# Performance work log

Measured on AMD Instinct MI355X. Metric: run time of the kernel, lower is better.

## Reference

```python
import jax, jax.numpy as jnp
import numpy as np

B, S, D = 4, 2048, 1024
H = 16
HD = D // H  # 64
FF = 4096


def setup_inputs() -> dict:
    key = jax.random.key(0)
    ks = jax.random.split(key, 11)
    sd = 1.0 / np.sqrt(D)
    inp = {
        "embeddings": jax.random.normal(ks[0], (B, S, D), dtype=jnp.float32),
        # per-head Linear weights stacked: [H, head_dim, D] (torch Linear layout)
        "Wq": jax.random.uniform(ks[1], (H, HD, D), jnp.float32, -sd, sd),
        "bq": jax.random.uniform(ks[2], (H, HD), jnp.float32, -sd, sd),
        "Wk": jax.random.uniform(ks[3], (H, HD, D), jnp.float32, -sd, sd),
        "bk": jax.random.uniform(ks[4], (H, HD), jnp.float32, -sd, sd),
        "Wv": jax.random.uniform(ks[5], (H, HD, D), jnp.float32, -sd, sd),
        "bv": jax.random.uniform(ks[6], (H, HD), jnp.float32, -sd, sd),
        "W1": jax.random.uniform(ks[7], (FF, D), jnp.float32, -sd, sd),
        "b1": jax.random.uniform(ks[8], (FF,), jnp.float32, -sd, sd),
        "W2": jax.random.uniform(ks[9], (D, FF), jnp.float32, -1.0 / np.sqrt(FF), 1.0 / np.sqrt(FF)),
        "b2": jax.random.uniform(ks[10], (D,), jnp.float32, -1.0 / np.sqrt(FF), 1.0 / np.sqrt(FF)),
    }
    return inp


def reference(embeddings, Wq, bq, Wk, bk, Wv, bv, W1, b1, W2, b2):
    # Per-head projections, batched over heads: [B,H,S,HD]
    Q = jnp.einsum("bsd,hed->bhse", embeddings, Wq) + bq[None, :, None, :]
    K = jnp.einsum("bsd,hed->bhse", embeddings, Wk) + bk[None, :, None, :]
    V = jnp.einsum("bsd,hed->bhse", embeddings, Wv) + bv[None, :, None, :]
    # NOTE: original scales by sqrt(embed_dim), not sqrt(head_dim)
    scale = 1.0 / jnp.sqrt(jnp.asarray(D, embeddings.dtype))
    scores = jnp.einsum("bhse,bhte->bhst", Q, K) * scale  # [B,H,S,S]
    A = jax.nn.softmax(scores, axis=-1)
    Hh = jnp.einsum("bhst,bhte->bhse", A, V)  # [B,H,S,HD]
    # concat heads along last dim (head order matches torch.cat)
    Hcat = jnp.transpose(Hh, (0, 2, 1, 3)).reshape(B, S, D)
    hid = jax.nn.relu(Hcat @ W1.T + b1)
    return hid @ W2.T + b2
```

## Files before the change

kernel.cpp:

```cpp
#include <hip/hip_runtime.h>
#include <stdint.h>


typedef __attribute__((ext_vector_type(8))) short bf16x8;
typedef __attribute__((ext_vector_type(4))) float f32x4;

__device__ __forceinline__ float bf2f(unsigned short u) {
  union { float f; uint32_t i; } v; v.i = ((uint32_t)u) << 16; return v.f;
}
__device__ __forceinline__ unsigned short f2bf(float f) {
  union { float f; uint32_t i; } v; v.f = f;
  uint32_t i = v.i;
  return (unsigned short)((i + 0x7fffu + ((i >> 16) & 1u)) >> 16);
}

#if __has_builtin(__builtin_amdgcn_exp2f)
#define EXP2(x) __builtin_amdgcn_exp2f(x)
#else
#define EXP2(x) __expf((x) * 0.6931471805599453f)
#endif

__device__ __forceinline__ uint32_t cvtpk(float p0, float p1) {
  uint32_t r;
  asm("v_cvt_pk_bf16_f32 %0, %1, %2" : "=v"(r) : "v"(p0), "v"(p1));
  return r;
}

__device__ __forceinline__ void gld16(const void* g, void* l) {
  __builtin_amdgcn_global_load_lds(
      (const __attribute__((address_space(1))) uint32_t*)(uintptr_t)g,
      (__attribute__((address_space(3))) uint32_t*)(uintptr_t)l, 16, 0, 0);
}

#define SCALE_Q 0.04508422002778011f

#define W1B          0
#define W2B    4194304
#define B1B    8388608
#define B2B    8392704
#define BQB    8393728
#define BKB    8394752
#define BVB    8395776
#define EMBB   8396800
#define WQB   16785408
#define WKB   17833984
#define WVB   18882560
#define QOFF  19931136
#define KOFF  28319744
#define VTOFF 36708352
#define HCOFF 45096960
#define HIDOFF 8396800

__global__ void cvt_all(const float* __restrict__ emb, const float* __restrict__ Wq,
                        const float* __restrict__ bq,  const float* __restrict__ Wk,
                        const float* __restrict__ bk,  const float* __restrict__ Wv,
                        const float* __restrict__ bv,  const float* __restrict__ W1,
                        const float* __restrict__ b1,  const float* __restrict__ W2,
                        const float* __restrict__ b2,  unsigned short* __restrict__ ws) {
  const int i4 = blockIdx.x * 256 + threadIdx.x;
  if (i4 >= 4982784) return;
  const float* s; unsigned short* d; int base;
  if      (i4 < 2097152) { s = emb; d = ws + EMBB; base = 0; }
  else if (i4 < 2359296) { s = Wq;  d = ws + WQB;  base = 2097152; }
  else if (i4 < 2621440) { s = Wk;  d = ws + WKB;  base = 2359296; }
  else if (i4 < 2883584) { s = Wv;  d = ws + WVB;  base = 2621440; }
  else if (i4 < 3932160) { s = W1;  d = ws + W1B;  base = 2883584; }
  else if (i4 < 4980736) { s = W2;  d = ws + W2B;  base = 3932160; }
  else if (i4 < 4980992) { s = bq;  d = ws + BQB;  base = 4980736; }
  else if (i4 < 4981248) { s = bk;  d = ws + BKB;  base = 4980992; }
  else if (i4 < 4981504) { s = bv;  d = ws + BVB;  base = 4981248; }
  else if (i4 < 4982528) { s = b1;  d = ws + B1B;  base = 4981504; }
  else                   { s = b2;  d = ws + B2B;  base = 4982528; }
  const int j = i4 - base;
  const float4 v = ((const float4*)s)[j];
  ushort4 o;
  o.x = f2bf(v.x); o.y = f2bf(v.y); o.z = f2bf(v.z); o.w = f2bf(v.w);
  *(ushort4*)(d + (size_t)j * 4) = o;
}

template <int MODE>
__launch_bounds__(256, 4)
__global__ void gemm128(const unsigned short* __restrict__ A,
                        const unsigned short* __restrict__ W0,
                        const unsigned short* __restrict__ W1p,
                        const unsigned short* __restrict__ W2p,
                        const unsigned short* __restrict__ bias0,
                        const unsigned short* __restrict__ bias1,
                        const unsigned short* __restrict__ bias2,
                        unsigned short* __restrict__ out0,
                        unsigned short* __restrict__ out1,
                        unsigned short* __restrict__ out2,
                        float* __restrict__ foutp,
                        int N, int K) {
  __shared__ unsigned short At[128 * 64];
  __shared__ unsigned short Bt[128 * 64];
  const int tid  = threadIdx.x;
  const int wave = tid >> 6, lane = tid & 63;
  const int quad = lane >> 4, l15 = lane & 15;

  const int lid = blockIdx.x + blockIdx.y * gridDim.x;
  const int s_ = lid >> 3;
  const int rowBase = (((lid & 7) + ((s_ & 7) << 3)) << 7);
  const int colBase = ((s_ >> 3) << 7);

  const unsigned short* W = W0;
  const unsigned short* bias = bias0;
  int colW = colBase;
  if (MODE == 2) {
    const int which = colBase >> 10;
    if (which == 1) { W = W1p; bias = bias1; }
    if (which == 2) { W = W2p; bias = bias2; }
    colW = colBase & 1023;
  }

  const unsigned short* gA[4]; const unsigned short* gB[4];
  unsigned short *lA[4], *lB[4];
#pragma unroll
  for (int i = 0; i < 4; ++i) {
    const int u = tid + 256 * i;
    const int r = u >> 3, e = (((u & 7) ^ (r & 7)) * 8);
    gA[i] = A + (size_t)(rowBase + r) * K + e;
    gB[i] = W + (size_t)(colW + r) * K + e;
    lA[i] = At + u * 8;
    lB[i] = Bt + u * 8;
  }

  const int wrow = (wave & 1) * 64, wcol = (wave >> 1) * 64;
  int aoff[2][4], boff[2][4];
#pragma unroll
  for (int kk = 0; kk < 2; ++kk)
#pragma unroll
    for (int t = 0; t < 4; ++t) {
      const int ra = wrow + t * 16 + l15;
      aoff[kk][t] = ra * 64 + (((quad + 4 * kk) ^ (ra & 7)) * 8);
      const int rb = wcol + t * 16 + l15;
      boff[kk][t] = rb * 64 + (((quad + 4 * kk) ^ (rb & 7)) * 8);
    }

  f32x4 acc[4][4] = {};
  for (int k0 = 0; k0 < K; k0 += 64) {
    __syncthreads();
#pragma unroll
    for (int i = 0; i < 4; ++i) { gld16(gA[i], lA[i]); gld16(gB[i], lB[i]); }
#pragma unroll
    for (int i = 0; i < 4; ++i) { gA[i] += 64; gB[i] += 64; }
    __syncthreads();
#pragma unroll
    for (int kk = 0; kk < 2; ++kk) {
      bf16x8 af[4], bfr[4];
#pragma unroll
      for (int t = 0; t < 4; ++t) af[t]  = *(const bf16x8*)(At + aoff[kk][t]);
#pragma unroll
      for (int t = 0; t < 4; ++t) bfr[t] = *(const bf16x8*)(Bt + boff[kk][t]);
#pragma unroll
      for (int mt = 0; mt < 4; ++mt)
#pragma unroll
        for (int nt = 0; nt < 4; ++nt)
          acc[mt][nt] = __builtin_amdgcn_mfma_f32_16x16x32_bf16(
              af[mt], bfr[nt], acc[mt][nt], 0, 0, 0);
    }
  }

#pragma unroll
  for (int mt = 0; mt < 4; ++mt) {
    const int row = rowBase + wrow + mt * 16 + quad * 4;
#pragma unroll
    for (int nt = 0; nt < 4; ++nt) {
      const int cIn = colW + wcol + nt * 16 + l15;
      const float bv = bf2f(bias[cIn]);
      if (MODE == 2) {
        const int which = colBase >> 10;
        const int h = cIn >> 6, e = cIn & 63;
#pragma unroll
        for (int r = 0; r < 4; ++r) {
          const int tok = row + r;
          const int b = tok >> 11, s = tok & 2047;
          const float v = acc[mt][nt][r] + bv;
          const size_t bh = (size_t)(b * 16 + h);
          if (which == 0)      out0[(bh * 2048 + s) * 64 + e] = f2bf(v * SCALE_Q);
          else if (which == 1) out1[(bh * 2048 + s) * 64 + e] = f2bf(v);
          else                 out2[(bh * 64 + e) * 2048 + s] = f2bf(v);
        }
      } else if (MODE == 1) {
#pragma unroll
        for (int r = 0; r < 4; ++r) {
          const float v = fmaxf(acc[mt][nt][r] + bv, 0.0f);
          out0[(size_t)(row + r) * N + cIn] = f2bf(v);
        }
      } else {
#pragma unroll
        for (int r = 0; r < 4; ++r)
          foutp[(size_t)(row + r) * N + cIn] = acc[mt][nt][r] + bv;
      }
    }
  }
}

__launch_bounds__(256, 4)
__global__ void flash_attn(const unsigned short* __restrict__ Q,
                           const unsigned short* __restrict__ Kg,
                           const unsigned short* __restrict__ Vt,
                           unsigned short* __restrict__ Hc) {
  __shared__ unsigned short Kt[2 * 64 * 64];
  __shared__ unsigned short Vs[64 * 64];
  __shared__ unsigned short Pl[4][32 * 64];
  const int tid  = threadIdx.x;
  const int wave = tid >> 6, lane = tid & 63;
  const int quad = lane >> 4, l15 = lane & 15;

  const int lid = blockIdx.x + blockIdx.y * gridDim.x;
  const int s_ = lid >> 3;
  const int bh = (lid & 7) + ((s_ & 7) << 3);
  const int q0 = ((s_ >> 3) << 7) + wave * 32;

  const size_t base = (size_t)bh * (2048 * 64);
  const unsigned short* Qb = Q  + base;
  const unsigned short* Kb = Kg + base;
  const unsigned short* Vb = Vt + base;

  bf16x8 qf[2][2];
#pragma unroll
  for (int qt = 0; qt < 2; ++qt) {
    const int q = q0 + qt * 16 + l15;
#pragma unroll
    for (int kk = 0; kk < 2; ++kk)
      qf[qt][kk] = *(const bf16x8*)(Qb + (size_t)q * 64 + kk * 32 + quad * 8);
  }

  const int u0 = tid, u1 = tid + 256;
  const int kr0 = u0 >> 3, kc0 = (((u0 & 7) ^ (kr0 & 7)) * 8);
  const int kr1 = u1 >> 3, kc1 = (((u1 & 7) ^ (kr1 & 7)) * 8);
  const unsigned short* gK0 = Kb + (size_t)kr0 * 64 + kc0;
  const unsigned short* gK1 = Kb + (size_t)kr1 * 64 + kc1;
  const unsigned short* gV0 = Vb + (size_t)kr0 * 2048 + kc0;
  const unsigned short* gV1 = Vb + (size_t)kr1 * 2048 + kc1;
  unsigned short* lK0 = Kt + u0 * 8;
  unsigned short* lK1 = Kt + u1 * 8;
  unsigned short* lV0 = Vs + u0 * 8;
  unsigned short* lV1 = Vs + u1 * 8;

  gld16(gK0, lK0); gld16(gK1, lK1);
  gld16(gV0, lV0); gld16(gV1, lV1);
  gK0 += 4096; gK1 += 4096; gV0 += 64; gV1 += 64;
  __syncthreads();

  const short oneb = (short)0x3F80;
  const bf16x8 ones = {oneb, oneb, oneb, oneb, oneb, oneb, oneb, oneb};
  f32x4 o[2][4] = {};
  f32x4 lacc[2] = {};
  unsigned short* Pw = Pl[wave];

  for (int it = 0; it < 32; ++it) {
    const int nb = ((it + 1) & 1) * 4096;
    gld16(gK0, lK0 + nb); gld16(gK1, lK1 + nb);
    gK0 += 4096; gK1 += 4096;

    const unsigned short* Kc = Kt + (it & 1) * 4096;

    f32x4 st[4][2] = {};
    __builtin_amdgcn_s_setprio(1);
#pragma unroll
    for (int tt = 0; tt < 4; ++tt) {
      const int t = tt * 16 + l15;
      const bf16x8 kf0 = *(const bf16x8*)(Kc + t * 64 + ((quad       ^ (t & 7)) * 8));
      const bf16x8 kf1 = *(const bf16x8*)(Kc + t * 64 + (((quad + 4) ^ (t & 7)) * 8));
#pragma unroll
      for (int qt = 0; qt < 2; ++qt) {
        st[tt][qt] = __builtin_amdgcn_mfma_f32_16x16x32_bf16(kf0, qf[qt][0], st[tt][qt], 0, 0, 0);
        st[tt][qt] = __builtin_amdgcn_mfma_f32_16x16x32_bf16(kf1, qf[qt][1], st[tt][qt], 0, 0, 0);
      }
    }
    __builtin_amdgcn_s_setprio(0);

#pragma unroll
    for (int tt = 0; tt < 4; ++tt) {
      const int tc = tt * 2 + (quad >> 1);
#pragma unroll
      for (int qt = 0; qt < 2; ++qt) {
        const float p0 = EXP2(st[tt][qt][0]);
        const float p1 = EXP2(st[tt][qt][1]);
        const float p2 = EXP2(st[tt][qt][2]);
        const float p3 = EXP2(st[tt][qt][3]);
        uint2 w;
        w.x = cvtpk(p0, p1);
        w.y = cvtpk(p2, p3);
        const int qrow = qt * 16 + l15;
        *(uint2*)(Pw + qrow * 64 + ((tc ^ (qrow & 7)) * 8) + (quad & 1) * 4) = w;
      }
    }

    asm volatile("s_waitcnt vmcnt(2)" ::: "memory");
    __builtin_amdgcn_s_barrier();

    bf16x8 pf[2][2];
#pragma unroll
    for (int mt = 0; mt < 2; ++mt) {
      const int qq = mt * 16 + l15;
      pf[mt][0] = *(const bf16x8*)(Pw + qq * 64 + ((quad       ^ (qq & 7)) * 8));
      pf[mt][1] = *(const bf16x8*)(Pw + qq * 64 + (((quad + 4) ^ (qq & 7)) * 8));
    }
    __builtin_amdgcn_s_setprio(1);
#pragma unroll
    for (int nt = 0; nt < 4; ++nt) {
      const int e = nt * 16 + l15;
      const bf16x8 vf0 = *(const bf16x8*)(Vs + e * 64 + ((quad       ^ (e & 7)) * 8));
      const bf16x8 vf1 = *(const bf16x8*)(Vs + e * 64 + (((quad + 4) ^ (e & 7)) * 8));
#pragma unroll
      for (int mt = 0; mt < 2; ++mt) {
        o[mt][nt] = __builtin_amdgcn_mfma_f32_16x16x32_bf16(pf[mt][0], vf0, o[mt][nt], 0, 0, 0);
        o[mt][nt] = __builtin_amdgcn_mfma_f32_16x16x32_bf16(pf[mt][1], vf1, o[mt][nt], 0, 0, 0);
      }
    }
#pragma unroll
    for (int mt = 0; mt < 2; ++mt) {
      lacc[mt] = __builtin_amdgcn_mfma_f32_16x16x32_bf16(pf[mt][0], ones, lacc[mt], 0, 0, 0);
      lacc[mt] = __builtin_amdgcn_mfma_f32_16x16x32_bf16(pf[mt][1], ones, lacc[mt], 0, 0, 0);
    }
    __builtin_amdgcn_s_setprio(0);

    asm volatile("s_waitcnt vmcnt(0)" ::: "memory");
    __builtin_amdgcn_s_barrier();

    if (it < 31) {
      gld16(gV0, lV0); gld16(gV1, lV1);
      gV0 += 64; gV1 += 64;
    }
  }

  const int b = bh >> 4, h = bh & 15;
#pragma unroll
  for (int mt = 0; mt < 2; ++mt)
#pragma unroll
    for (int r = 0; r < 4; ++r) {
      const int qg = q0 + mt * 16 + quad * 4 + r;
      const float inv = __builtin_amdgcn_rcpf(lacc[mt][r]);
#pragma unroll
      for (int nt = 0; nt < 4; ++nt) {
        const int e = nt * 16 + l15;
        Hc[((size_t)b * 2048 + qg) * 1024 + h * 64 + e] = f2bf(o[mt][nt][r] * inv);
      }
    }
}

extern "C" void kernel_launch(void* const* d_in, const int* in_sizes, int n_in,
                              void* d_out, int out_size, void* d_ws, size_t ws_size,
                              hipStream_t stream) {
  const float* emb = (const float*)d_in[0];
  const float* Wq  = (const float*)d_in[1];
  const float* bq  = (const float*)d_in[2];
  const float* Wk  = (const float*)d_in[3];
  const float* bk  = (const float*)d_in[4];
  const float* Wv  = (const float*)d_in[5];
  const float* bv  = (const float*)d_in[6];
  const float* W1  = (const float*)d_in[7];
  const float* b1  = (const float*)d_in[8];
  const float* W2  = (const float*)d_in[9];
  const float* b2  = (const float*)d_in[10];

  unsigned short* ws = (unsigned short*)d_ws;
  float* out = (float*)d_out;

  cvt_all<<<19465, 256, 0, stream>>>(emb, Wq, bq, Wk, bk, Wv, bv, W1, b1, W2, b2, ws);
  gemm128<2><<<dim3(24, 64), 256, 0, stream>>>(
      ws + EMBB, ws + WQB, ws + WKB, ws + WVB, ws + BQB, ws + BKB, ws + BVB,
      ws + QOFF, ws + KOFF, ws + VTOFF, nullptr, 3072, 1024);
  flash_attn<<<dim3(16, 64), 256, 0, stream>>>(ws + QOFF, ws + KOFF, ws + VTOFF, ws + HCOFF);
  gemm128<1><<<dim3(32, 64), 256, 0, stream>>>(
      ws + HCOFF, ws + W1B, nullptr, nullptr, ws + B1B, nullptr, nullptr,
      ws + HIDOFF, nullptr, nullptr, nullptr, 4096, 1024);
  gemm128<0><<<dim3(8, 64), 256, 0, stream>>>(
      ws + HIDOFF, ws + W2B, nullptr, nullptr, ws + B2B, nullptr, nullptr,
      nullptr, nullptr, nullptr, out, 1024, 4096);
}
```

Baseline: 404.4 us.

## Add 256x256 double-buffered GEMM kernel for QKV and FFN1 projections

Adds a new GEMM kernel with 256x256 output tiles, 512 threads and double-buffered LDS for the K loop. It replaces the 128-tile kernel for the QKV projection and the first FFN layer. Block ids are remapped so groups of 8 row tiles share column tiles. The goal is more data reuse per block and overlap of global loads with MFMA work. In exchange it uses more LDS and registers, lowers occupancy, and launches fewer blocks for the 256 CUs.

```diff
diff --git a/kernel.cpp b/kernel.cpp
--- a/kernel.cpp
+++ b/kernel.cpp
@@ -79,6 +79,150 @@
 }
 
 template <int MODE>
+__launch_bounds__(512, 2)
+__global__ void gemm256(const unsigned short* __restrict__ A,
+                        const unsigned short* __restrict__ W0,
+                        const unsigned short* __restrict__ W1p,
+                        const unsigned short* __restrict__ W2p,
+                        const unsigned short* __restrict__ bias0,
+                        const unsigned short* __restrict__ bias1,
+                        const unsigned short* __restrict__ bias2,
+                        unsigned short* __restrict__ out0,
+                        unsigned short* __restrict__ out1,
+                        unsigned short* __restrict__ out2,
+                        float* __restrict__ foutp,
+                        int N, int K) {
+  __shared__ unsigned short At[2 * 256 * 64];
+  __shared__ unsigned short Bt[2 * 256 * 64];
+  const int tid  = threadIdx.x;
+  const int wave = tid >> 6, lane = tid & 63;
+  const int quad = lane >> 4, l15 = lane & 15;
+  const int wm = wave >> 2, wn = wave & 3;
+
+  const int lid = blockIdx.x + blockIdx.y * gridDim.x;
+  const int s_ = lid >> 3;
+  const int rowBase = (((lid & 7) + ((s_ & 3) << 3)) << 8);
+  const int colBase = ((s_ >> 2) << 8);
+
+  const unsigned short* W = W0;
+  const unsigned short* bias = bias0;
+  int colW = colBase;
+  if (MODE == 2) {
+    const int which = colBase >> 10;
+    if (which == 1) { W = W1p; bias = bias1; }
+    if (which == 2) { W = W2p; bias = bias2; }
+    colW = colBase & 1023;
+  }
+
+  const unsigned short* gA[4]; const unsigned short* gB[4];
+  unsigned short *lA[4], *lB[4];
+#pragma unroll
+  for (int i = 0; i < 4; ++i) {
+    const int u = tid + 512 * i;
+    const int r = u >> 3, e = (((u & 7) ^ (r & 7)) * 8);
+    gA[i] = A + (size_t)(rowBase + r) * K + e;
+    gB[i] = W + (size_t)(colW + r) * K + e;
+    lA[i] = At + u * 8;
+    lB[i] = Bt + u * 8;
+  }
+
+  int aoff[8], boff[4];
+#pragma unroll
+  for (int mt = 0; mt < 8; ++mt) {
+    const int ra = wm * 128 + mt * 16 + l15;
+    aoff[mt] = ra * 64 + ((quad ^ (ra & 7)) * 8);
+  }
+#pragma unroll
+  for (int nt = 0; nt < 4; ++nt) {
+    const int rb = wn * 64 + nt * 16 + l15;
+    boff[nt] = rb * 64 + ((quad ^ (rb & 7)) * 8);
+  }
+
+#pragma unroll
+  for (int i = 0; i < 4; ++i) { gld16(gA[i], lA[i]); gld16(gB[i], lB[i]); }
+#pragma unroll
+  for (int i = 0; i < 4; ++i) { gA[i] += 64; gB[i] += 64; }
+#pragma unroll
+  for (int i = 0; i < 4; ++i) { gld16(gA[i], lA[i] + 16384); gld16(gB[i], lB[i] + 16384); }
+#pragma unroll
+  for (int i = 0; i < 4; ++i) { gA[i] += 64; gB[i] += 64; }
+  asm volatile("s_waitcnt vmcnt(8)" ::: "memory");
+  __builtin_amdgcn_s_barrier();
+
+  f32x4 acc[8][4] = {};
+  const int T = K >> 6;
+  for (int t = 0; t < T; ++t) {
+    const int cur = t & 1;
+    const unsigned short* Ab = At + (cur << 14);
+    const unsigned short* Bb = Bt + (cur << 14);
+#pragma unroll
+    for (int kk = 0; kk < 2; ++kk) {
+      const int kx = kk << 5;
+      bf16x8 af[8], bfr[4];
+#pragma unroll
+      for (int mt = 0; mt < 8; ++mt) af[mt]  = *(const bf16x8*)(Ab + (aoff[mt] ^ kx));
+#pragma unroll
+      for (int nt = 0; nt < 4; ++nt) bfr[nt] = *(const bf16x8*)(Bb + (boff[nt] ^ kx));
+      __builtin_amdgcn_s_setprio(1);
+#pragma unroll
+      for (int mt = 0; mt < 8; ++mt)
+#pragma unroll
+        for (int nt = 0; nt < 4; ++nt)
+          acc[mt][nt] = __builtin_amdgcn_mfma_f32_16x16x32_bf16(
+              af[mt], bfr[nt], acc[mt][nt], 0, 0, 0);
+      __builtin_amdgcn_s_setprio(0);
+    }
+    if (t == T - 1) break;
+    __builtin_amdgcn_s_barrier();
+    if (t + 2 < T) {
+      const int db = cur << 14;
+#pragma unroll
+      for (int i = 0; i < 4; ++i) { gld16(gA[i], lA[i] + db); gld16(gB[i], lB[i] + db); }
+#pragma unroll
+      for (int i = 0; i < 4; ++i) { gA[i] += 64; gB[i] += 64; }
+      asm volatile("s_waitcnt vmcnt(8)" ::: "memory");
+    } else {
+      asm volatile("s_waitcnt vmcnt(0)" ::: "memory");
+    }
+    __builtin_amdgcn_s_barrier();
+  }
+
+#pragma unroll
+  for (int mt = 0; mt < 8; ++mt) {
+    const int row = rowBase + wm * 128 + mt * 16 + quad * 4;
+#pragma unroll
+    for (int nt = 0; nt < 4; ++nt) {
+      const int cIn = colW + wn * 64 + nt * 16 + l15;
+      const float bv = bf2f(bias[cIn]);
+      if (MODE == 2) {
+        const int which = colBase >> 10;
+        const int h = cIn >> 6, e = cIn & 63;
+#pragma unroll
+        for (int r = 0; r < 4; ++r) {
+          const int tok = row + r;
+          const int b = tok >> 11, s = tok & 2047;
+          const float v = acc[mt][nt][r] + bv;
+          const size_t bh = (size_t)(b * 16 + h);
+          if (which == 0)      out0[(bh * 2048 + s) * 64 + e] = f2bf(v * SCALE_Q);
+          else if (which == 1) out1[(bh * 2048 + s) * 64 + e] = f2bf(v);
+          else                 out2[(bh * 64 + e) * 2048 + s] = f2bf(v);
+        }
+      } else if (MODE == 1) {
+#pragma unroll
+        for (int r = 0; r < 4; ++r) {
+          const float v = fmaxf(acc[mt][nt][r] + bv, 0.0f);
+          out0[(size_t)(row + r) * N + cIn] = f2bf(v);
+        }
+      } else {
+#pragma unroll
+        for (int r = 0; r < 4; ++r)
+          foutp[(size_t)(row + r) * N + cIn] = acc[mt][nt][r] + bv;
+      }
+    }
+  }
+}
+
+template <int MODE>
 __launch_bounds__(256, 4)
 __global__ void gemm128(const unsigned short* __restrict__ A,
                         const unsigned short* __restrict__ W0,
@@ -361,11 +505,11 @@
   float* out = (float*)d_out;
 
   cvt_all<<<19465, 256, 0, stream>>>(emb, Wq, bq, Wk, bk, Wv, bv, W1, b1, W2, b2, ws);
-  gemm128<2><<<dim3(24, 64), 256, 0, stream>>>(
+  gemm256<2><<<dim3(12, 32), 512, 0, stream>>>(
       ws + EMBB, ws + WQB, ws + WKB, ws + WVB, ws + BQB, ws + BKB, ws + BVB,
       ws + QOFF, ws + KOFF, ws + VTOFF, nullptr, 3072, 1024);
   flash_attn<<<dim3(16, 64), 256, 0, stream>>>(ws + QOFF, ws + KOFF, ws + VTOFF, ws + HCOFF);
-  gemm128<1><<<dim3(32, 64), 256, 0, stream>>>(
+  gemm256<1><<<dim3(16, 32), 512, 0, stream>>>(
       ws + HCOFF, ws + W1B, nullptr, nullptr, ws + B1B, nullptr, nullptr,
       ws + HIDOFF, nullptr, nullptr, nullptr, 4096, 1024);
   gemm128<0><<<dim3(8, 64), 256, 0, stream>>>(
```

New measurement: 435.8 us. 7.8% more time.
